# Kernel optimization log

Measured on AMD Instinct MI355X. Metric: run time of the kernel, lower is better.

The kernel has to match this reference:

```python
import jax, jax.numpy as jnp
import numpy as np
import math

B, TT, TS, C, H, L = 8, 256, 512, 512, 8, 10
HD = C // H
TOPK_FRAME = 64
# layer schedule mirrors MultimodalTransformer.forward tower order:
# 4 stimulus cross-attn (kv=frames, topk), 2 causal self-attn, 2 history cross-attn, 2 causal self-attn
# kv_source: 0=frames, 1=self, 2=id_prev
SCHED = [(0, False, TOPK_FRAME)] * 4 + [(1, True, None)] * 2 + [(2, False, None)] * 2 + [(1, True, None)] * 2


def setup_inputs() -> dict:
    key = jax.random.key(0)
    ks = jax.random.split(key, 4)
    kws = jax.random.split(ks[3], 6)
    w = lambda k, s: jax.random.normal(k, s, jnp.float32) * 0.02
    return {
        "id_x": jax.random.normal(ks[0], (B, TT, C), jnp.float32),
        "id_prev": jax.random.normal(ks[1], (B, TT, C), jnp.float32),
        "frames": jax.random.normal(ks[2], (B, TS, C), jnp.float32),
        "Wq": w(kws[0], (L, C, C)), "bq": jnp.zeros((L, C), jnp.float32),
        "Wk": w(kws[1], (L, C, C)), "bk": jnp.zeros((L, C), jnp.float32),
        "Wv": w(kws[2], (L, C, C)), "bv": jnp.zeros((L, C), jnp.float32),
        "Wo": w(kws[3], (L, C, C)), "bo": jnp.zeros((L, C), jnp.float32),
        "W1": w(kws[4], (L, C, 4 * C)), "b1": jnp.zeros((L, 4 * C), jnp.float32),
        "W2": w(kws[5], (L, 4 * C, C)), "b2": jnp.zeros((L, C), jnp.float32),
        "ln1_g": jnp.ones((L, C), jnp.float32), "ln1_b": jnp.zeros((L, C), jnp.float32),
        "ln2_g": jnp.ones((L, C), jnp.float32), "ln2_b": jnp.zeros((L, C), jnp.float32),
        "lnf_g": jnp.ones((L, C), jnp.float32), "lnf_b": jnp.zeros((L, C), jnp.float32),
    }


def _ln(x, g, b):
    mu = x.mean(-1, keepdims=True)
    var = ((x - mu) ** 2).mean(-1, keepdims=True)
    return (x - mu) * jax.lax.rsqrt(var + 1e-5) * g + b


def _block(x, kv, causal, topk, p):
    # Block.forward: x = x + attn(ln1(x), kv, kv, mask); x = x + mlp(ln2(x)); return ln_f(x)
    Wq, bq, Wk, bk, Wv, bv, Wo, bo, W1, b1, W2, b2, l1g, l1b, l2g, l2b, lfg, lfb = p
    Bx, Tt, Cx = x.shape
    Ts = kv.shape[1]
    h = _ln(x, l1g, l1b)
    q = (h @ Wq + bq).reshape(Bx, Tt, H, HD).transpose(0, 2, 1, 3)   # [B,H,Tt,HD]
    k = (kv @ Wk + bk).reshape(Bx, Ts, H, HD).transpose(0, 2, 1, 3)  # [B,H,Ts,HD]
    v = (kv @ Wv + bv).reshape(Bx, Ts, H, HD).transpose(0, 2, 1, 3)
    att = jnp.einsum('bhqd,bhkd->bhqk', q, k) * (1.0 / math.sqrt(HD))
    if causal:
        m = jnp.tril(jnp.ones((Tt, Ts), dtype=bool))
        att = jnp.where(m, att, -jnp.inf)
    if topk is not None and topk < Ts:
        top = jax.lax.top_k(att, topk)[0]           # [B,H,Tt,topk]
        att = jnp.where(att < top[..., -1:], -jnp.inf, att)
    w_att = jax.nn.softmax(att, axis=-1)
    y = jnp.einsum('bhqk,bhkd->bhqd', w_att, v).transpose(0, 2, 1, 3).reshape(Bx, Tt, Cx)
    x = x + y @ Wo + bo
    h2 = _ln(x, l2g, l2b)
    x = x + jax.nn.gelu(h2 @ W1 + b1, approximate=False) @ W2 + b2
    return _ln(x, lfg, lfb)


def _forward(id_x, id_prev, frames, Wq, bq, Wk, bk, Wv, bv, Wo, bo, W1, b1, W2, b2,
             ln1_g, ln1_b, ln2_g, ln2_b, lnf_g, lnf_b):
    x = id_x
    for i, (src, causal, topk) in enumerate(SCHED):
        kv = (frames, x, id_prev)[src]
        p = (Wq[i], bq[i], Wk[i], bk[i], Wv[i], bv[i], Wo[i], bo[i],
             W1[i], b1[i], W2[i], b2[i],
             ln1_g[i], ln1_b[i], ln2_g[i], ln2_b[i], lnf_g[i], lnf_b[i])
        x = _block(x, kv, causal, topk, p)
    return x


def reference(id_x, id_prev, frames, Wq, bq, Wk, bk, Wv, bv, Wo, bo, W1, b1, W2, b2,
              ln1_g, ln1_b, ln2_g, ln2_b, lnf_g, lnf_b):
    return _forward(id_x, id_prev, frames, Wq, bq, Wk, bk, Wv, bv, Wo, bo, W1, b1, W2, b2,
                    ln1_g, ln1_b, ln2_g, ln2_b, lnf_g, lnf_b)
```

## Files before the change

kernel.cpp:

```cpp
#include <hip/hip_runtime.h>
#include <math.h>

#define CC 512
#define NH 8
#define HD 64
#define TT 256

typedef __attribute__((ext_vector_type(8))) short short8v;
typedef __attribute__((ext_vector_type(4))) float f32x4;

__device__ inline unsigned short bfc(float f) {
  unsigned u = __float_as_uint(f);
  return (unsigned short)((u + 0x7fffu + ((u >> 16) & 1u)) >> 16);
}
__device__ inline float b2f(unsigned short s) {
  return __uint_as_float((unsigned)s << 16);
}
__device__ inline void gld16(const void* g, void* l) {
  __builtin_amdgcn_global_load_lds(
      (const __attribute__((address_space(1))) unsigned int*)g,
      (__attribute__((address_space(3))) unsigned int*)l, 16, 0, 0);
}

__global__ __launch_bounds__(256) void prep_k(const float* __restrict__ id_x,
    const float* __restrict__ frames, const float* __restrict__ id_prev,
    float* __restrict__ x, unsigned short* __restrict__ fb,
    unsigned short* __restrict__ pb) {
  int i = blockIdx.x * 256 + threadIdx.x;
  if (i < 262144) {
    ((float4*)x)[i] = ((const float4*)id_x)[i];
  } else if (i < 786432) {
    int j = i - 262144;
    float4 f = ((const float4*)frames)[j];
    ushort4 o; o.x = bfc(f.x); o.y = bfc(f.y); o.z = bfc(f.z); o.w = bfc(f.w);
    ((ushort4*)fb)[j] = o;
  } else {
    int j = i - 786432;
    float4 f = ((const float4*)id_prev)[j];
    ushort4 o; o.x = bfc(f.x); o.y = bfc(f.y); o.z = bfc(f.z); o.w = bfc(f.w);
    ((ushort4*)pb)[j] = o;
  }
}

__global__ __launch_bounds__(256) void ln_bf(const float* __restrict__ in,
    unsigned short* __restrict__ out, const float* __restrict__ g, const float* __restrict__ b) {
  int row = (blockIdx.x << 2) + (threadIdx.x >> 6), lane = threadIdx.x & 63;
  const float* r = in + (size_t)row * CC;
  float4 v0 = *(const float4*)(r + (lane << 2));
  float4 v1 = *(const float4*)(r + 256 + (lane << 2));
  float s = v0.x + v0.y + v0.z + v0.w + v1.x + v1.y + v1.z + v1.w;
  #pragma unroll
  for (int o = 32; o; o >>= 1) s += __shfl_xor(s, o);
  float mu = s * (1.0f / CC);
  float d0x = v0.x - mu, d0y = v0.y - mu, d0z = v0.z - mu, d0w = v0.w - mu;
  float d1x = v1.x - mu, d1y = v1.y - mu, d1z = v1.z - mu, d1w = v1.w - mu;
  float sq = d0x*d0x + d0y*d0y + d0z*d0z + d0w*d0w + d1x*d1x + d1y*d1y + d1z*d1z + d1w*d1w;
  #pragma unroll
  for (int o = 32; o; o >>= 1) sq += __shfl_xor(sq, o);
  float inv = rsqrtf(sq * (1.0f / CC) + 1e-5f);
  float4 g0 = *(const float4*)(g + (lane << 2)), g1 = *(const float4*)(g + 256 + (lane << 2));
  float4 b0 = *(const float4*)(b + (lane << 2)), b1 = *(const float4*)(b + 256 + (lane << 2));
  ushort4 o0, o1;
  o0.x = bfc(d0x*inv*g0.x + b0.x); o0.y = bfc(d0y*inv*g0.y + b0.y);
  o0.z = bfc(d0z*inv*g0.z + b0.z); o0.w = bfc(d0w*inv*g0.w + b0.w);
  o1.x = bfc(d1x*inv*g1.x + b1.x); o1.y = bfc(d1y*inv*g1.y + b1.y);
  o1.z = bfc(d1z*inv*g1.z + b1.z); o1.w = bfc(d1w*inv*g1.w + b1.w);
  *(ushort4*)(out + (size_t)row * CC + (lane << 2)) = o0;
  *(ushort4*)(out + (size_t)row * CC + 256 + (lane << 2)) = o1;
}

__global__ __launch_bounds__(256) void ln_final(const float* __restrict__ in,
    float* __restrict__ out, const float* __restrict__ g, const float* __restrict__ b) {
  int row = (blockIdx.x << 2) + (threadIdx.x >> 6), lane = threadIdx.x & 63;
  const float* r = in + (size_t)row * CC;
  float4 v0 = *(const float4*)(r + (lane << 2));
  float4 v1 = *(const float4*)(r + 256 + (lane << 2));
  float s = v0.x + v0.y + v0.z + v0.w + v1.x + v1.y + v1.z + v1.w;
  #pragma unroll
  for (int o = 32; o; o >>= 1) s += __shfl_xor(s, o);
  float mu = s * (1.0f / CC);
  float d0x = v0.x - mu, d0y = v0.y - mu, d0z = v0.z - mu, d0w = v0.w - mu;
  float d1x = v1.x - mu, d1y = v1.y - mu, d1z = v1.z - mu, d1w = v1.w - mu;
  float sq = d0x*d0x + d0y*d0y + d0z*d0z + d0w*d0w + d1x*d1x + d1y*d1y + d1z*d1z + d1w*d1w;
  #pragma unroll
  for (int o = 32; o; o >>= 1) sq += __shfl_xor(sq, o);
  float inv = rsqrtf(sq * (1.0f / CC) + 1e-5f);
  float4 g0 = *(const float4*)(g + (lane << 2)), g1 = *(const float4*)(g + 256 + (lane << 2));
  float4 b0 = *(const float4*)(b + (lane << 2)), b1 = *(const float4*)(b + 256 + (lane << 2));
  float4 o0, o1;
  o0.x = d0x*inv*g0.x + b0.x; o0.y = d0y*inv*g0.y + b0.y;
  o0.z = d0z*inv*g0.z + b0.z; o0.w = d0w*inv*g0.w + b0.w;
  o1.x = d1x*inv*g1.x + b1.x; o1.y = d1y*inv*g1.y + b1.y;
  o1.z = d1z*inv*g1.z + b1.z; o1.w = d1w*inv*g1.w + b1.w;
  *(float4*)(out + (size_t)row * CC + (lane << 2)) = o0;
  *(float4*)(out + (size_t)row * CC + 256 + (lane << 2)) = o1;
}

__global__ __launch_bounds__(256) void ln_chain(const float* __restrict__ in,
    float* __restrict__ xout, unsigned short* __restrict__ xb,
    const float* __restrict__ gf, const float* __restrict__ bf,
    const float* __restrict__ g1, const float* __restrict__ b1,
    unsigned short* __restrict__ hout) {
  int row = (blockIdx.x << 2) + (threadIdx.x >> 6), lane = threadIdx.x & 63;
  const float* r = in + (size_t)row * CC;
  float4 v0 = *(const float4*)(r + (lane << 2));
  float4 v1 = *(const float4*)(r + 256 + (lane << 2));
  float s = v0.x + v0.y + v0.z + v0.w + v1.x + v1.y + v1.z + v1.w;
  #pragma unroll
  for (int o = 32; o; o >>= 1) s += __shfl_xor(s, o);
  float mu = s * (1.0f / CC);
  float d0x = v0.x - mu, d0y = v0.y - mu, d0z = v0.z - mu, d0w = v0.w - mu;
  float d1x = v1.x - mu, d1y = v1.y - mu, d1z = v1.z - mu, d1w = v1.w - mu;
  float sq = d0x*d0x + d0y*d0y + d0z*d0z + d0w*d0w + d1x*d1x + d1y*d1y + d1z*d1z + d1w*d1w;
  #pragma unroll
  for (int o = 32; o; o >>= 1) sq += __shfl_xor(sq, o);
  float inv = rsqrtf(sq * (1.0f / CC) + 1e-5f);
  float4 g0 = *(const float4*)(gf + (lane << 2)), g1v = *(const float4*)(gf + 256 + (lane << 2));
  float4 b0 = *(const float4*)(bf + (lane << 2)), b1v = *(const float4*)(bf + 256 + (lane << 2));
  float4 x0, x1;
  x0.x = d0x*inv*g0.x + b0.x; x0.y = d0y*inv*g0.y + b0.y;
  x0.z = d0z*inv*g0.z + b0.z; x0.w = d0w*inv*g0.w + b0.w;
  x1.x = d1x*inv*g1v.x + b1v.x; x1.y = d1y*inv*g1v.y + b1v.y;
  x1.z = d1z*inv*g1v.z + b1v.z; x1.w = d1w*inv*g1v.w + b1v.w;
  *(float4*)(xout + (size_t)row * CC + (lane << 2)) = x0;
  *(float4*)(xout + (size_t)row * CC + 256 + (lane << 2)) = x1;
  ushort4 xb0, xb1;
  xb0.x = bfc(x0.x); xb0.y = bfc(x0.y); xb0.z = bfc(x0.z); xb0.w = bfc(x0.w);
  xb1.x = bfc(x1.x); xb1.y = bfc(x1.y); xb1.z = bfc(x1.z); xb1.w = bfc(x1.w);
  *(ushort4*)(xb + (size_t)row * CC + (lane << 2)) = xb0;
  *(ushort4*)(xb + (size_t)row * CC + 256 + (lane << 2)) = xb1;
  float s2 = x0.x + x0.y + x0.z + x0.w + x1.x + x1.y + x1.z + x1.w;
  #pragma unroll
  for (int o = 32; o; o >>= 1) s2 += __shfl_xor(s2, o);
  float mu2 = s2 * (1.0f / CC);
  float e0x = x0.x - mu2, e0y = x0.y - mu2, e0z = x0.z - mu2, e0w = x0.w - mu2;
  float e1x = x1.x - mu2, e1y = x1.y - mu2, e1z = x1.z - mu2, e1w = x1.w - mu2;
  float sq2 = e0x*e0x + e0y*e0y + e0z*e0z + e0w*e0w + e1x*e1x + e1y*e1y + e1z*e1z + e1w*e1w;
  #pragma unroll
  for (int o = 32; o; o >>= 1) sq2 += __shfl_xor(sq2, o);
  float inv2 = rsqrtf(sq2 * (1.0f / CC) + 1e-5f);
  float4 h0 = *(const float4*)(g1 + (lane << 2)), h1 = *(const float4*)(g1 + 256 + (lane << 2));
  float4 c0 = *(const float4*)(b1 + (lane << 2)), c1 = *(const float4*)(b1 + 256 + (lane << 2));
  ushort4 ho0, ho1;
  ho0.x = bfc(e0x*inv2*h0.x + c0.x); ho0.y = bfc(e0y*inv2*h0.y + c0.y);
  ho0.z = bfc(e0z*inv2*h0.z + c0.z); ho0.w = bfc(e0w*inv2*h0.w + c0.w);
  ho1.x = bfc(e1x*inv2*h1.x + c1.x); ho1.y = bfc(e1y*inv2*h1.y + c1.y);
  ho1.z = bfc(e1z*inv2*h1.z + c1.z); ho1.w = bfc(e1w*inv2*h1.w + c1.w);
  *(ushort4*)(hout + (size_t)row * CC + (lane << 2)) = ho0;
  *(ushort4*)(hout + (size_t)row * CC + 256 + (lane << 2)) = ho1;
}

__global__ __launch_bounds__(256) void transpose_w(
    const float* __restrict__ Wq, const float* __restrict__ Wk,
    const float* __restrict__ Wv, const float* __restrict__ Wo,
    const float* __restrict__ W1, const float* __restrict__ W2,
    int layer_base, unsigned short* __restrict__ wT) {
  int lz = blockIdx.x / 3072;
  int layer = layer_base + lz;
  int bid = blockIdx.x - lz * 3072;
  unsigned short* wTl = wT + (size_t)lz * 3145728;
  const float* src; unsigned short* dst; int R, Cn, tile, lg;
  if (bid < 1024) {
    int seg = bid >> 8; tile = bid & 255; R = 512; Cn = 512; lg = 4;
    const float* s4[4] = {Wq, Wk, Wv, Wo};
    src = s4[seg] + (size_t)layer * 262144;
    dst = wTl + (size_t)seg * 262144;
  } else if (bid < 2048) {
    tile = bid - 1024; R = 512; Cn = 2048; lg = 6;
    src = W1 + (size_t)layer * 1048576; dst = wTl + 1048576;
  } else {
    tile = bid - 2048; R = 2048; Cn = 512; lg = 4;
    src = W2 + (size_t)layer * 1048576; dst = wTl + 2097152;
  }
  int trb = tile >> lg, tcb = tile & ((1 << lg) - 1);
  __shared__ float tl[32][33];
  int t = threadIdx.x;
  int r = t >> 3, c4 = (t & 7) << 2;
  const float* sp = src + (size_t)(trb * 32 + r) * Cn + tcb * 32 + c4;
  float4 fv = *(const float4*)sp;
  tl[r][c4] = fv.x; tl[r][c4 + 1] = fv.y; tl[r][c4 + 2] = fv.z; tl[r][c4 + 3] = fv.w;
  __syncthreads();
  unsigned short* dp = dst + (size_t)(tcb * 32 + r) * R + trb * 32 + c4;
  ushort4 ov;
  ov.x = bfc(tl[c4][r]); ov.y = bfc(tl[c4 + 1][r]);
  ov.z = bfc(tl[c4 + 2][r]); ov.w = bfc(tl[c4 + 3][r]);
  *(ushort4*)dp = ov;
}

template<int BM, int GELU, int RES, int OUTBF, int BIAS2, int QSC>
__global__ __launch_bounds__(256) void gemm_bf(
    const unsigned short* __restrict__ A, const unsigned short* __restrict__ WT,
    const float* __restrict__ bias, const float* __restrict__ bias2,
    void* __restrict__ outp, const float* __restrict__ res, int M, int N, int K) {
  __shared__ __align__(16) unsigned short As[2][BM * 64];
  __shared__ __align__(16) unsigned short Bs[2][64 * 64];
  const int tid = threadIdx.x, lane = tid & 63, wid = tid >> 6;
  const int bm = blockIdx.y * BM, bn = blockIdx.x << 6;
  const int wm = (wid >> 1) * (BM / 2), wn = (wid & 1) << 5;
  constexpr int MF = BM / 32;
  f32x4 acc[MF][2] = {};
  const int fr = lane & 15, fq = lane >> 4;
  const int srow_a = tid >> 3, sgc = tid & 7;

  auto stage = [&](int buf, int k0) {
    #pragma unroll
    for (int i = 0; i < BM / 32; i++) {
      int row = srow_a + (i << 5);
      int gcs = sgc ^ (row & 7);
      gld16(A + (size_t)(bm + row) * K + k0 + (gcs << 3),
            (char*)As[buf] + (i << 12) + (wid << 10));
    }
    #pragma unroll
    for (int i = 0; i < 2; i++) {
      int row = srow_a + (i << 5);
      int gcs = sgc ^ (row & 7);
      gld16(WT + (size_t)(bn + row) * K + k0 + (gcs << 3),
            (char*)Bs[buf] + (i << 12) + (wid << 10));
    }
  };

  stage(0, 0);
  __syncthreads();
  int cur = 0;
  for (int k0 = 0; k0 < K; k0 += 64) {
    if (k0 + 64 < K) stage(cur ^ 1, k0 + 64);
    short8v af[MF][2], bf2[2][2];
    #pragma unroll
    for (int mf = 0; mf < MF; mf++)
      #pragma unroll
      for (int ks = 0; ks < 2; ks++) {
        int r = wm + mf * 16 + fr;
        int c = (ks << 2) + fq;
        af[mf][ks] = *(const short8v*)((const char*)As[cur] + ((((r << 7) + (c << 4))) ^ ((r & 7) << 4)));
      }
    #pragma unroll
    for (int nf = 0; nf < 2; nf++)
      #pragma unroll
      for (int ks = 0; ks < 2; ks++) {
        int r = wn + nf * 16 + fr;
        int c = (ks << 2) + fq;
        bf2[nf][ks] = *(const short8v*)((const char*)Bs[cur] + ((((r << 7) + (c << 4))) ^ ((r & 7) << 4)));
      }
    #pragma unroll
    for (int mf = 0; mf < MF; mf++)
      #pragma unroll
      for (int nf = 0; nf < 2; nf++) {
        acc[mf][nf] = __builtin_amdgcn_mfma_f32_16x16x32_bf16(af[mf][0], bf2[nf][0], acc[mf][nf], 0, 0, 0);
        acc[mf][nf] = __builtin_amdgcn_mfma_f32_16x16x32_bf16(af[mf][1], bf2[nf][1], acc[mf][nf], 0, 0, 0);
      }
    __syncthreads();
    cur ^= 1;
  }
  #pragma unroll
  for (int mf = 0; mf < MF; mf++)
    #pragma unroll
    for (int nf = 0; nf < 2; nf++) {
      int col = bn + wn + nf * 16 + fr;
      float bia = (BIAS2 && col >= 512) ? bias2[col - 512] : bias[col];
      #pragma unroll
      for (int rr = 0; rr < 4; rr++) {
        int row = bm + wm + mf * 16 + fq * 4 + rr;
        float vv = acc[mf][nf][rr] + bia;
        if (GELU) vv = 0.5f * vv * (1.0f + erff(vv * 0.70710678118654752f));
        if (RES)  vv += res[(size_t)row * N + col];
        if (QSC)  vv *= 0.125f;
        if (OUTBF) ((unsigned short*)outp)[(size_t)row * N + col] = bfc(vv);
        else       ((float*)outp)[(size_t)row * N + col] = vv;
      }
    }
}

__global__ __launch_bounds__(256) void gemm_qkv(
    const unsigned short* __restrict__ hb, const unsigned short* __restrict__ wqT,
    const float* __restrict__ bq,
    const unsigned short* __restrict__ kvA, const unsigned short* __restrict__ wkvT,
    const float* __restrict__ bk, const float* __restrict__ bv,
    unsigned short* __restrict__ qout, unsigned short* __restrict__ kvout) {
  const int tid = threadIdx.x, lane = tid & 63, wid = tid >> 6;
  int bid = blockIdx.x;
  const unsigned short *A, *WT;
  const float *bias, *bias2;
  unsigned short* outp;
  int bm, bn, N;
  bool isq = bid < 256;
  if (isq) {
    A = hb; WT = wqT; bias = bq; bias2 = bq; outp = qout; N = 512;
    bm = (bid >> 3) << 6; bn = (bid & 7) << 6;
  } else {
    int t = bid - 256;
    A = kvA; WT = wkvT; bias = bk; bias2 = bv; outp = kvout; N = 1024;
    bm = (t >> 4) << 6; bn = (t & 15) << 6;
  }
  __shared__ __align__(16) unsigned short As[2][64 * 64];
  __shared__ __align__(16) unsigned short Bs[2][64 * 64];
  const int wm = (wid >> 1) << 5, wn = (wid & 1) << 5;
  f32x4 acc[2][2] = {};
  const int fr = lane & 15, fq = lane >> 4;
  const int srow_a = tid >> 3, sgc = tid & 7;
  auto stage = [&](int buf, int k0) {
    #pragma unroll
    for (int i = 0; i < 2; i++) {
      int row = srow_a + (i << 5);
      int gcs = sgc ^ (row & 7);
      gld16(A + (size_t)(bm + row) * 512 + k0 + (gcs << 3),
            (char*)As[buf] + (i << 12) + (wid << 10));
      gld16(WT + (size_t)(bn + row) * 512 + k0 + (gcs << 3),
            (char*)Bs[buf] + (i << 12) + (wid << 10));
    }
  };
  stage(0, 0);
  __syncthreads();
  int cur = 0;
  for (int k0 = 0; k0 < 512; k0 += 64) {
    if (k0 + 64 < 512) stage(cur ^ 1, k0 + 64);
    short8v af[2][2], bf2[2][2];
    #pragma unroll
    for (int mf = 0; mf < 2; mf++)
      #pragma unroll
      for (int ks = 0; ks < 2; ks++) {
        int r = wm + mf * 16 + fr;
        int c = (ks << 2) + fq;
        af[mf][ks] = *(const short8v*)((const char*)As[cur] + ((((r << 7) + (c << 4))) ^ ((r & 7) << 4)));
        int r2 = wn + mf * 16 + fr;
        bf2[mf][ks] = *(const short8v*)((const char*)Bs[cur] + ((((r2 << 7) + (c << 4))) ^ ((r2 & 7) << 4)));
      }
    #pragma unroll
    for (int mf = 0; mf < 2; mf++)
      #pragma unroll
      for (int nf = 0; nf < 2; nf++) {
        acc[mf][nf] = __builtin_amdgcn_mfma_f32_16x16x32_bf16(af[mf][0], bf2[nf][0], acc[mf][nf], 0, 0, 0);
        acc[mf][nf] = __builtin_amdgcn_mfma_f32_16x16x32_bf16(af[mf][1], bf2[nf][1], acc[mf][nf], 0, 0, 0);
      }
    __syncthreads();
    cur ^= 1;
  }
  #pragma unroll
  for (int mf = 0; mf < 2; mf++)
    #pragma unroll
    for (int nf = 0; nf < 2; nf++) {
      int col = bn + wn + nf * 16 + fr;
      float bia = (col >= 512) ? bias2[col - 512] : bias[col];
      #pragma unroll
      for (int rr = 0; rr < 4; rr++) {
        int row = bm + wm + mf * 16 + fq * 4 + rr;
        float vv = acc[mf][nf][rr] + bia;
        if (isq) vv *= 0.125f;
        outp[(size_t)row * N + col] = bfc(vv);
      }
    }
}

template<int CAUSAL, int TOPK, int TSK>
__global__ __launch_bounds__(512, 4) void attn_m(
    const unsigned short* __restrict__ qb, const unsigned short* __restrict__ kv,
    unsigned short* __restrict__ yb) {
  constexpr int NT = TSK / 64;
  constexpr int NKC = TSK / 128;
  constexpr int SST = TSK + 8;
  __shared__ float S[8 * SST];
  __shared__ __align__(16) unsigned short Ks[128 * 64];
  __shared__ __align__(16) unsigned short Qs[16 * 64];
  __shared__ float swt[TOPK ? 8 : 1][TOPK ? 128 : 1];
  __shared__ unsigned short kidx[TOPK ? 8 : 1][TOPK ? 128 : 1];
  int tid = threadIdx.x, lane = tid & 63, wid = tid >> 6;
  int bid = blockIdx.x;
  int swz = ((bid & 7) << 8) | (bid >> 3);
  int b = swz >> 8, h = (swz >> 5) & 7, q0 = (swz & 31) << 3;
  if (tid < 64) {
    int row = tid >> 3, sp = tid & 7;
    gld16(qb + (size_t)((b << 8) + q0 + row) * CC + (h << 6) + ((sp ^ (row & 7)) << 3),
          (char*)Qs);
  } else if (tid < 128) {
    short8v z = {0, 0, 0, 0, 0, 0, 0, 0};
    *(short8v*)((char*)Qs + (tid << 4)) = z;
  }
  __syncthreads();
  short8v aF[2];
  {
    int r = lane & 15, kq2 = lane >> 4;
    #pragma unroll
    for (int kc2 = 0; kc2 < 2; kc2++)
      aF[kc2] = *(const short8v*)((const char*)Qs +
                 (((r << 7) + (kc2 << 6) + (kq2 << 4)) ^ ((r & 7) << 4)));
  }
  int nte = NKC;
  if (CAUSAL) { int ub = (q0 + 8 + 127) >> 7; nte = ub < NKC ? ub : NKC; }
  const unsigned short* kgb = kv + (size_t)b * TSK * 1024 + (h << 6);
  for (int t = 0; t < nte; t++) {
    __syncthreads();
    #pragma unroll
    for (int j = 0; j < 2; j++) {
      int s = (wid << 7) + (j << 6) + lane;
      int row = s >> 3, sp = s & 7;
      gld16(kgb + (size_t)((t << 7) + row) * 1024 + ((sp ^ (row & 7)) << 3),
            (char*)Ks + (wid << 11) + (j << 10));
    }
    __syncthreads();
    int kq2 = lane >> 4;
    f32x4 acc = {};
    int key16 = (wid << 4) + (lane & 15);
    #pragma unroll
    for (int kc2 = 0; kc2 < 2; kc2++) {
      short8v bF = *(const short8v*)((const char*)Ks +
                    (((key16 << 7) + (kc2 << 6) + (kq2 << 4)) ^ ((key16 & 7) << 4)));
      acc = __builtin_amdgcn_mfma_f32_16x16x32_bf16(aF[kc2], bF, acc, 0, 0, 0);
    }
    if (kq2 < 2) {
      int col = (t << 7) + key16;
      #pragma unroll
      for (int r = 0; r < 4; r++)
        S[(kq2 * 4 + r) * SST + col] = acc[r];
    }
  }
  __syncthreads();
  int row = wid;
  int qi = q0 + row;
  int jmax = CAUSAL ? (qi + 1) : TSK;
  const unsigned short* vgb = kv + (size_t)b * TSK * 1024 + 512 + (h << 6) + lane;
  float sc[NT];
  float lmax = -3.0e38f;
  #pragma unroll
  for (int tt = 0; tt < NT; tt++) {
    int key = lane + (tt << 6);
    float v = (!CAUSAL || key < jmax) ? S[row * SST + key] : -3.0e38f;
    sc[tt] = v;
    lmax = fmaxf(lmax, v);
  }
  float mx = lmax;
  #pragma unroll
  for (int o = 32; o; o >>= 1) mx = fmaxf(mx, __shfl_xor(mx, o));
  float oacc = 0.f;
  if (TOPK) {
    unsigned key[NT];
    #pragma unroll
    for (int tt = 0; tt < NT; tt++) {
      unsigned u = __float_as_uint(sc[tt]);
      key[tt] = (u & 0x80000000u) ? ~u : (u | 0x80000000u);
    }
    unsigned prefix = 0u;
    for (int bit = 31; bit >= 0; bit--) {
      unsigned cand = prefix | (1u << bit);
      int cnt = 0;
      #pragma unroll
      for (int tt = 0; tt < NT; tt++)
        cnt += __popcll(__ballot(key[tt] >= cand));
      if (cnt >= 64) {
        prefix = cand;
        if (cnt == 64) break;
      }
    }
    float wvv[NT];
    float psum = 0.f;
    int basec = 0;
    #pragma unroll
    for (int tt = 0; tt < NT; tt++) {
      bool keep = key[tt] >= prefix;
      float wv = keep ? exp2f((sc[tt] - mx) * 1.4426950408889634f) : 0.f;
      wvv[tt] = wv;
      psum += wv;
      unsigned long long mask = __ballot(keep);
      if (keep) {
        int pos = basec + (int)__popcll(mask & ((1ull << lane) - 1ull));
        if (pos < 128) {
          kidx[row][pos] = (unsigned short)(lane + (tt << 6));
          swt[row][pos] = wv;
        }
      }
      basec += (int)__popcll(mask);
    }
    #pragma unroll
    for (int o = 32; o; o >>= 1) psum += __shfl_xor(psum, o);
    float inv = 1.0f / psum;
    int nk = basec;
    if (nk <= 128) {
      float a0 = 0.f, a1 = 0.f, a2 = 0.f, a3 = 0.f;
      int i = 0;
      for (; i + 3 < nk; i += 4) {
        a0 += swt[row][i]     * b2f(vgb[(size_t)kidx[row][i] * 1024]);
        a1 += swt[row][i + 1] * b2f(vgb[(size_t)kidx[row][i + 1] * 1024]);
        a2 += swt[row][i + 2] * b2f(vgb[(size_t)kidx[row][i + 2] * 1024]);
        a3 += swt[row][i + 3] * b2f(vgb[(size_t)kidx[row][i + 3] * 1024]);
      }
      for (; i < nk; i++) a0 += swt[row][i] * b2f(vgb[(size_t)kidx[row][i] * 1024]);
      oacc = (a0 + a1 + a2 + a3) * inv;
    } else {
      #pragma unroll
      for (int tt = 0; tt < NT; tt++)
        S[row * SST + lane + (tt << 6)] = wvv[tt];
      float a0 = 0.f, a1 = 0.f;
      for (int j = 0; j + 1 < TSK; j += 2) {
        a0 += S[row * SST + j]     * b2f(vgb[(size_t)j * 1024]);
        a1 += S[row * SST + j + 1] * b2f(vgb[(size_t)(j + 1) * 1024]);
      }
      oacc = (a0 + a1) * inv;
    }
  } else {
    float psum = 0.f;
    #pragma unroll
    for (int tt = 0; tt < NT; tt++) {
      int keyj = lane + (tt << 6);
      float wv = (keyj < jmax) ? exp2f((sc[tt] - mx) * 1.4426950408889634f) : 0.f;
      S[row * SST + keyj] = wv;
      psum += wv;
    }
    #pragma unroll
    for (int o = 32; o; o >>= 1) psum += __shfl_xor(psum, o);
    float inv = 1.0f / psum;
    float a0 = 0.f, a1 = 0.f, a2 = 0.f, a3 = 0.f;
    int j = 0;
    for (; j + 3 < jmax; j += 4) {
      a0 += S[row * SST + j]     * b2f(vgb[(size_t)j * 1024]);
      a1 += S[row * SST + j + 1] * b2f(vgb[(size_t)(j + 1) * 1024]);
      a2 += S[row * SST + j + 2] * b2f(vgb[(size_t)(j + 2) * 1024]);
      a3 += S[row * SST + j + 3] * b2f(vgb[(size_t)(j + 3) * 1024]);
    }
    for (; j < jmax; j++) a0 += S[row * SST + j] * b2f(vgb[(size_t)j * 1024]);
    oacc = (a0 + a1 + a2 + a3) * inv;
  }
  yb[(size_t)((b << 8) + qi) * CC + (h << 6) + lane] = bfc(oacc);
}

extern "C" void kernel_launch(void* const* d_in, const int* in_sizes, int n_in,
                              void* d_out, int out_size, void* d_ws, size_t ws_size,
                              hipStream_t stream) {
  const float* id_x    = (const float*)d_in[0];
  const float* id_prev = (const float*)d_in[1];
  const float* frames  = (const float*)d_in[2];
  const float* Wq = (const float*)d_in[3];  const float* bq = (const float*)d_in[4];
  const float* Wk = (const float*)d_in[5];  const float* bk = (const float*)d_in[6];
  const float* Wv = (const float*)d_in[7];  const float* bv = (const float*)d_in[8];
  const float* Wo = (const float*)d_in[9];  const float* bo = (const float*)d_in[10];
  const float* W1 = (const float*)d_in[11]; const float* b1 = (const float*)d_in[12];
  const float* W2 = (const float*)d_in[13]; const float* b2 = (const float*)d_in[14];
  const float* l1g = (const float*)d_in[15]; const float* l1b = (const float*)d_in[16];
  const float* l2g = (const float*)d_in[17]; const float* l2b = (const float*)d_in[18];
  const float* lfg = (const float*)d_in[19]; const float* lfb = (const float*)d_in[20];

  float* x = (float*)d_out;
  char* W  = (char*)d_ws;
  unsigned short* qbuf = (unsigned short*)W;
  unsigned short* kvb  = (unsigned short*)(W + ((size_t)4  << 20));
  unsigned short* m1b  = (unsigned short*)(W + ((size_t)4  << 20));
  unsigned short* hb   = (unsigned short*)(W + ((size_t)12 << 20));
  unsigned short* ybf  = (unsigned short*)(W + ((size_t)14 << 20));
  unsigned short* xb   = (unsigned short*)(W + ((size_t)16 << 20));
  unsigned short* fb   = (unsigned short*)(W + ((size_t)18 << 20));
  unsigned short* pb   = (unsigned short*)(W + ((size_t)22 << 20));
  unsigned short* wT   = (unsigned short*)(W + ((size_t)24 << 20));

  const bool allw = ws_size >= (((size_t)24 << 20) + (size_t)10 * 3145728 * 2);

  prep_k<<<4096, 256, 0, stream>>>(id_x, frames, id_prev, x, fb, pb);
  if (allw)
    transpose_w<<<30720, 256, 0, stream>>>(Wq, Wk, Wv, Wo, W1, W2, 0, wT);

  static const int ssrc[10] = {0, 0, 0, 0, 1, 1, 2, 2, 1, 1};

  for (int i = 0; i < 10; i++) {
    if (!allw)
      transpose_w<<<3072, 256, 0, stream>>>(Wq, Wk, Wv, Wo, W1, W2, i, wT);
    unsigned short* wTl = wT + (allw ? (size_t)i * 3145728 : 0);
    unsigned short* wqT = wTl;
    unsigned short* wkvT = wTl + 262144;
    unsigned short* woT = wTl + 786432;
    unsigned short* w1T = wTl + 1048576;
    unsigned short* w2T = wTl + 2097152;

    if (i == 0)
      ln_bf<<<512, 256, 0, stream>>>(x, hb, l1g, l1b);

    const unsigned short* kvsrc; int Mkv;
    if (ssrc[i] == 0)      { kvsrc = fb; Mkv = 4096; }
    else if (ssrc[i] == 1) { kvsrc = xb; Mkv = 2048; }
    else                   { kvsrc = pb; Mkv = 2048; }
    gemm_qkv<<<256 + (Mkv / 64) * 16, 256, 0, stream>>>(
        hb, wqT, bq + i * 512, kvsrc, wkvT, bk + i * 512, bv + i * 512, qbuf, kvb);

    if (ssrc[i] == 0)      attn_m<0, 1, 512><<<2048, 512, 0, stream>>>(qbuf, kvb, ybf);
    else if (ssrc[i] == 1) attn_m<1, 0, 256><<<2048, 512, 0, stream>>>(qbuf, kvb, ybf);
    else                   attn_m<0, 0, 256><<<2048, 512, 0, stream>>>(qbuf, kvb, ybf);

    gemm_bf<32, 0, 1, 0, 0, 0><<<dim3(8, 64), 256, 0, stream>>>(ybf, woT, bo + i * 512, nullptr, x, x, 2048, 512, 512);
    ln_bf<<<512, 256, 0, stream>>>(x, hb, l2g + i * 512, l2b + i * 512);
    gemm_bf<128, 1, 0, 1, 0, 0><<<dim3(32, 16), 256, 0, stream>>>(hb, w1T, b1 + i * 2048, nullptr, m1b, nullptr, 2048, 2048, 512);
    gemm_bf<32, 0, 1, 0, 0, 0><<<dim3(8, 64), 256, 0, stream>>>(m1b, w2T, b2 + i * 512, nullptr, x, x, 2048, 512, 2048);

    if (i < 9)
      ln_chain<<<512, 256, 0, stream>>>(x, x, xb, lfg + i * 512, lfb + i * 512,
                                        l1g + (i + 1) * 512, l1b + (i + 1) * 512, hb);
    else
      ln_final<<<512, 256, 0, stream>>>(x, x, lfg + i * 512, lfb + i * 512);
  }
}
```

Before: 1.011 ms.

## Load attention Q/K fragments directly from global and batch weight-transpose tiles

Result: no change. 1.026 ms (+1.4%).

```diff
diff --git a/kernel.cpp b/kernel.cpp
--- a/kernel.cpp
+++ b/kernel.cpp
@@ -155,36 +155,49 @@
     const float* __restrict__ Wv, const float* __restrict__ Wo,
     const float* __restrict__ W1, const float* __restrict__ W2,
     int layer_base, unsigned short* __restrict__ wT) {
-  int lz = blockIdx.x / 3072;
+  int lz = blockIdx.x / 768;
   int layer = layer_base + lz;
-  int bid = blockIdx.x - lz * 3072;
+  int bid = blockIdx.x - lz * 768;
   unsigned short* wTl = wT + (size_t)lz * 3145728;
-  const float* src; unsigned short* dst; int R, Cn, tile, lg;
-  if (bid < 1024) {
-    int seg = bid >> 8; tile = bid & 255; R = 512; Cn = 512; lg = 4;
+  const float* src; unsigned short* dst; int R, Cn, trb, tcg;
+  if (bid < 256) {
+    int seg = bid >> 6, t4 = bid & 63;
+    R = 512; Cn = 512;
     const float* s4[4] = {Wq, Wk, Wv, Wo};
     src = s4[seg] + (size_t)layer * 262144;
     dst = wTl + (size_t)seg * 262144;
-  } else if (bid < 2048) {
-    tile = bid - 1024; R = 512; Cn = 2048; lg = 6;
+    trb = t4 >> 2; tcg = t4 & 3;
+  } else if (bid < 512) {
+    int t4 = bid - 256;
+    R = 512; Cn = 2048;
     src = W1 + (size_t)layer * 1048576; dst = wTl + 1048576;
+    trb = t4 >> 4; tcg = t4 & 15;
   } else {
-    tile = bid - 2048; R = 2048; Cn = 512; lg = 4;
+    int t4 = bid - 512;
+    R = 2048; Cn = 512;
     src = W2 + (size_t)layer * 1048576; dst = wTl + 2097152;
-  }
-  int trb = tile >> lg, tcb = tile & ((1 << lg) - 1);
-  __shared__ float tl[32][33];
+    trb = t4 >> 2; tcg = t4 & 3;
+  }
+  __shared__ float tl[4][32][33];
   int t = threadIdx.x;
   int r = t >> 3, c4 = (t & 7) << 2;
-  const float* sp = src + (size_t)(trb * 32 + r) * Cn + tcb * 32 + c4;
-  float4 fv = *(const float4*)sp;
-  tl[r][c4] = fv.x; tl[r][c4 + 1] = fv.y; tl[r][c4 + 2] = fv.z; tl[r][c4 + 3] = fv.w;
+  #pragma unroll
+  for (int u = 0; u < 4; u++) {
+    int tcb = (tcg << 2) + u;
+    float4 fv = *(const float4*)(src + (size_t)(trb * 32 + r) * Cn + tcb * 32 + c4);
+    tl[u][r][c4] = fv.x; tl[u][r][c4 + 1] = fv.y;
+    tl[u][r][c4 + 2] = fv.z; tl[u][r][c4 + 3] = fv.w;
+  }
   __syncthreads();
-  unsigned short* dp = dst + (size_t)(tcb * 32 + r) * R + trb * 32 + c4;
-  ushort4 ov;
-  ov.x = bfc(tl[c4][r]); ov.y = bfc(tl[c4 + 1][r]);
-  ov.z = bfc(tl[c4 + 2][r]); ov.w = bfc(tl[c4 + 3][r]);
-  *(ushort4*)dp = ov;
+  #pragma unroll
+  for (int u = 0; u < 4; u++) {
+    int tcb = (tcg << 2) + u;
+    unsigned short* dp = dst + (size_t)(tcb * 32 + r) * R + trb * 32 + c4;
+    ushort4 ov;
+    ov.x = bfc(tl[u][c4][r]); ov.y = bfc(tl[u][c4 + 1][r]);
+    ov.z = bfc(tl[u][c4 + 2][r]); ov.w = bfc(tl[u][c4 + 3][r]);
+    *(ushort4*)dp = ov;
+  }
 }
 
 template<int BM, int GELU, int RES, int OUTBF, int BIAS2, int QSC>
@@ -355,58 +368,40 @@
     const unsigned short* __restrict__ qb, const unsigned short* __restrict__ kv,
     unsigned short* __restrict__ yb) {
   constexpr int NT = TSK / 64;
-  constexpr int NKC = TSK / 128;
+  constexpr int NKG = TSK / 16;
   constexpr int SST = TSK + 8;
   __shared__ float S[8 * SST];
-  __shared__ __align__(16) unsigned short Ks[128 * 64];
-  __shared__ __align__(16) unsigned short Qs[16 * 64];
   __shared__ float swt[TOPK ? 8 : 1][TOPK ? 128 : 1];
   __shared__ unsigned short kidx[TOPK ? 8 : 1][TOPK ? 128 : 1];
   int tid = threadIdx.x, lane = tid & 63, wid = tid >> 6;
   int bid = blockIdx.x;
   int swz = ((bid & 7) << 8) | (bid >> 3);
   int b = swz >> 8, h = (swz >> 5) & 7, q0 = (swz & 31) << 3;
-  if (tid < 64) {
-    int row = tid >> 3, sp = tid & 7;
-    gld16(qb + (size_t)((b << 8) + q0 + row) * CC + (h << 6) + ((sp ^ (row & 7)) << 3),
-          (char*)Qs);
-  } else if (tid < 128) {
-    short8v z = {0, 0, 0, 0, 0, 0, 0, 0};
-    *(short8v*)((char*)Qs + (tid << 4)) = z;
-  }
-  __syncthreads();
+  const int fr = lane & 15, kq2 = lane >> 4;
   short8v aF[2];
   {
-    int r = lane & 15, kq2 = lane >> 4;
-    #pragma unroll
-    for (int kc2 = 0; kc2 < 2; kc2++)
-      aF[kc2] = *(const short8v*)((const char*)Qs +
-                 (((r << 7) + (kc2 << 6) + (kq2 << 4)) ^ ((r & 7) << 4)));
-  }
-  int nte = NKC;
-  if (CAUSAL) { int ub = (q0 + 8 + 127) >> 7; nte = ub < NKC ? ub : NKC; }
+    short8v z = {0, 0, 0, 0, 0, 0, 0, 0};
+    #pragma unroll
+    for (int kc2 = 0; kc2 < 2; kc2++) {
+      aF[kc2] = z;
+      if (fr < 8)
+        aF[kc2] = *(const short8v*)(qb + (size_t)((b << 8) + q0 + fr) * CC +
+                                    (h << 6) + (kc2 << 5) + (kq2 << 3));
+    }
+  }
+  int nkg = NKG;
+  if (CAUSAL) { int ub = (q0 + 8 + 15) >> 4; nkg = ub < NKG ? ub : NKG; }
   const unsigned short* kgb = kv + (size_t)b * TSK * 1024 + (h << 6);
-  for (int t = 0; t < nte; t++) {
-    __syncthreads();
-    #pragma unroll
-    for (int j = 0; j < 2; j++) {
-      int s = (wid << 7) + (j << 6) + lane;
-      int row = s >> 3, sp = s & 7;
-      gld16(kgb + (size_t)((t << 7) + row) * 1024 + ((sp ^ (row & 7)) << 3),
-            (char*)Ks + (wid << 11) + (j << 10));
-    }
-    __syncthreads();
-    int kq2 = lane >> 4;
+  for (int kg = wid; kg < nkg; kg += 8) {
     f32x4 acc = {};
-    int key16 = (wid << 4) + (lane & 15);
     #pragma unroll
     for (int kc2 = 0; kc2 < 2; kc2++) {
-      short8v bF = *(const short8v*)((const char*)Ks +
-                    (((key16 << 7) + (kc2 << 6) + (kq2 << 4)) ^ ((key16 & 7) << 4)));
+      short8v bF = *(const short8v*)(kgb + (size_t)((kg << 4) + fr) * 1024 +
+                                     (kc2 << 5) + (kq2 << 3));
       acc = __builtin_amdgcn_mfma_f32_16x16x32_bf16(aF[kc2], bF, acc, 0, 0, 0);
     }
     if (kq2 < 2) {
-      int col = (t << 7) + key16;
+      int col = (kg << 4) + fr;
       #pragma unroll
       for (int r = 0; r < 4; r++)
         S[(kq2 * 4 + r) * SST + col] = acc[r];
@@ -552,13 +547,13 @@
 
   prep_k<<<4096, 256, 0, stream>>>(id_x, frames, id_prev, x, fb, pb);
   if (allw)
-    transpose_w<<<30720, 256, 0, stream>>>(Wq, Wk, Wv, Wo, W1, W2, 0, wT);
+    transpose_w<<<7680, 256, 0, stream>>>(Wq, Wk, Wv, Wo, W1, W2, 0, wT);
 
   static const int ssrc[10] = {0, 0, 0, 0, 1, 1, 2, 2, 1, 1};
 
   for (int i = 0; i < 10; i++) {
     if (!allw)
-      transpose_w<<<3072, 256, 0, stream>>>(Wq, Wk, Wv, Wo, W1, W2, i, wT);
+      transpose_w<<<768, 256, 0, stream>>>(Wq, Wk, Wv, Wo, W1, W2, i, wT);
     unsigned short* wTl = wT + (allw ? (size_t)i * 3145728 : 0);
     unsigned short* wqT = wTl;
     unsigned short* wkvT = wTl + 262144;
```
